# Optimization experiments

Measured on AMD Instinct MI355X. Metric: run time of the kernel, lower is better.

The kernel has to match this reference:

```python
import jax, jax.numpy as jnp
import numpy as np

N_NODES = 100000
N_EDGES = 1600000
IN_FEATS = 128
HID = 128
OUT_FEATS = 64


def setup_inputs() -> dict:
    key = jax.random.key(0)
    ks = jax.random.split(key, 8)
    node_ids = jnp.arange(N_NODES, dtype=jnp.int64)
    src = jax.random.randint(ks[0], (N_EDGES,), 0, N_NODES, dtype=jnp.int64)
    dst = jax.random.randint(ks[1], (N_EDGES,), 0, N_NODES, dtype=jnp.int64)
    emb = jax.random.normal(ks[2], (N_NODES, IN_FEATS), dtype=jnp.float32)
    W1 = jax.random.normal(ks[3], (IN_FEATS, HID), dtype=jnp.float32) / np.sqrt(IN_FEATS)
    b1 = jnp.zeros((HID,), dtype=jnp.float32)
    W2 = jax.random.normal(ks[4], (HID, OUT_FEATS), dtype=jnp.float32) / np.sqrt(HID)
    b2 = jnp.zeros((OUT_FEATS,), dtype=jnp.float32)
    return {"node_ids": node_ids, "src": src, "dst": dst, "emb": emb,
            "W1": W1, "b1": b1, "W2": W2, "b2": b2}


def _sym_norms(src, dst):
    # DGL GraphConv norm='both': D_out^{-1/2} on source side, D_in^{-1/2} on dest side,
    # degrees clamped to >= 1.
    ones = jnp.ones(src.shape[0], dtype=jnp.float32)
    deg_out = jax.ops.segment_sum(ones, src, num_segments=N_NODES)
    deg_in = jax.ops.segment_sum(ones, dst, num_segments=N_NODES)
    norm_src = jnp.clip(deg_out, 1.0, None) ** -0.5  # [N]
    norm_dst = jnp.clip(deg_in, 1.0, None) ** -0.5   # [N]
    return norm_src, norm_dst


def _spmm(src, dst, h):
    # rst[dst] += h[src]  (sparse adjacency aggregation)
    return jax.ops.segment_sum(h[src], dst, num_segments=N_NODES)


def reference(node_ids, src, dst, emb, W1, b1, W2, b2):
    norm_src, norm_dst = _sym_norms(src, dst)
    h = emb[node_ids]                                   # [N, IN]
    # Layer 1 (IN -> HID, relu): weight applied after aggregation (in <= out)
    h = _spmm(src, dst, h * norm_src[:, None]) * norm_dst[:, None]
    h = jax.nn.relu(h @ W1 + b1)                        # [N, HID]
    # Dropout(0.5) is identity in eval mode.
    # Layer 2 (HID -> OUT): DGL applies weight BEFORE aggregation when in > out
    h = (h @ W2) * norm_src[:, None]                    # [N, OUT]
    h = _spmm(src, dst, h) * norm_dst[:, None] + b2
    return h
```

## Files before the change

kernel.cpp:

```cpp
#include <hip/hip_runtime.h>

#define N_N 100000
#define N_E 1600000
#define SLOTS 48
#define N_PAD 100096

#define BK_SHIFT 8
#define BK_SIZE 256
#define NBKT 391
#define MAXB 5120
#define EPB2 4096
#define NBLK2 ((N_E + EPB2 - 1) / EPB2)
#define EPT 16

#define EMBB 6250
#define WB 96

typedef unsigned short ushort_t;
typedef unsigned int uint_t;
typedef _Float16 f16x8 __attribute__((ext_vector_type(8)));
typedef float f32x4 __attribute__((ext_vector_type(4)));

__device__ __forceinline__ ushort_t f2h(float f) {
    union { _Float16 h; ushort_t u; } c; c.h = (_Float16)f; return c.u;
}

__device__ __forceinline__ void acc2h(uint_t v, float wv, float& a, float& b) {
    union { uint_t u; _Float16 h[2]; } c; c.u = v;
    a = fmaf((float)c.h[0], wv, a);
    b = fmaf((float)c.h[1], wv, b);
}

__device__ __forceinline__ void addh(uint_t v, float& a, float& b) {
    union { uint_t u; _Float16 h[2]; } c; c.u = v;
    a += (float)c.h[0];
    b += (float)c.h[1];
}

__device__ __forceinline__ uint_t packh2(float a, float b) {
    union { _Float16 h[2]; uint_t u; } p;
    p.h[0] = (_Float16)a; p.h[1] = (_Float16)b;
    return p.u;
}

__global__ void __launch_bounds__(256) k_scatter_prep(
        const int* __restrict__ src, const int* __restrict__ dst,
        int* __restrict__ cur_d, int* __restrict__ cur_s,
        uint_t* __restrict__ pe_dst, uint_t* __restrict__ pe_src,
        const float* __restrict__ emb, ushort_t* __restrict__ embf,
        const float* __restrict__ W1, const float* __restrict__ W2,
        ushort_t* __restrict__ w1f, ushort_t* __restrict__ w2f) {
    int t = threadIdx.x, blk = blockIdx.x;
    if (blk >= NBLK2) {
        int pb = blk - NBLK2;
        if (pb < EMBB) {
            int i = pb * 512 + t;
            const float4* E4 = (const float4*)emb;
            ushort4* O4 = (ushort4*)embf;
            float4 v0 = E4[i], v1 = E4[i + 256];
            ushort4 o0, o1;
            o0.x = f2h(v0.x); o0.y = f2h(v0.y); o0.z = f2h(v0.z); o0.w = f2h(v0.w);
            o1.x = f2h(v1.x); o1.y = f2h(v1.y); o1.z = f2h(v1.z); o1.w = f2h(v1.w);
            O4[i] = o0; O4[i + 256] = o1;
        } else {
            int idx = (pb - EMBB) * 256 + t;
            int j = idx & 7, l = (idx >> 3) & 63;
            int k = (l >> 4) * 8 + j;
            int n = l & 15;
            if (idx < 16384) {
                int kc = (idx >> 9) & 3, nt = idx >> 11;
                w1f[idx] = f2h(W1[(kc * 32 + k) * 128 + nt * 16 + n]);
            } else {
                int i2 = idx - 16384;
                int kc = (i2 >> 9) & 3, nt = i2 >> 11;
                w2f[i2] = f2h(W2[(kc * 32 + k) * 64 + nt * 16 + n]);
            }
        }
        return;
    }
    __shared__ int cnt_[NBKT], lb_[NBKT], gb_[NBKT], cur_[NBKT];
    __shared__ int ps[512];
    __shared__ uint_t rec[EPB2];
    int e0 = blk * EPB2;
    for (int side = 0; side < 2; side++) {
        const int* key = side ? src : dst;
        for (int i = t; i < NBKT; i += 256) { cnt_[i] = 0; cur_[i] = 0; }
        __syncthreads();
        for (int i = 0; i < EPT; i++) {
            int e = e0 + t + i * 256;
            if (e < N_E) atomicAdd(&cnt_[key[e] >> BK_SHIFT], 1);
        }
        __syncthreads();
        ps[t] = (t < NBKT) ? cnt_[t] : 0;
        ps[t + 256] = (t + 256 < NBKT) ? cnt_[t + 256] : 0;
        __syncthreads();
        for (int d = 1; d < 512; d <<= 1) {
            int v0 = (t >= d) ? ps[t - d] : 0;
            int v1 = ps[t + 256 - d];
            __syncthreads();
            ps[t] += v0; ps[t + 256] += v1;
            __syncthreads();
        }
        int* curg = side ? cur_s : cur_d;
        for (int b = t; b < NBKT; b += 256) {
            int c = cnt_[b];
            lb_[b] = ps[b] - c;
            gb_[b] = c ? atomicAdd(&curg[b], c) : 0;
        }
        __syncthreads();
        for (int i = 0; i < EPT; i++) {
            int e = e0 + t + i * 256;
            if (e < N_E) {
                int s = src[e];
                int k = side ? s : dst[e];
                int b = k >> BK_SHIFT;
                int p = atomicAdd(&cur_[b], 1);
                rec[lb_[b] + p] = side ? (uint_t)s
                                       : ((uint_t)s | ((uint_t)(k & 255) << 17));
            }
        }
        __syncthreads();
        uint_t* pe = side ? pe_src : pe_dst;
        int wv = t >> 6, ln = t & 63, sub = ln >> 4, lj = ln & 15;
        for (int b0 = wv * 4; b0 < NBKT; b0 += 16) {
            int b = b0 + sub;
            if (b < NBKT) {
                int c = cnt_[b], lb = lb_[b], gb = gb_[b];
                for (int j = lj; j < c; j += 16)
                    if (gb + j < MAXB) pe[(size_t)b * MAXB + gb + j] = rec[lb + j];
            }
        }
        __syncthreads();
    }
}

__global__ void __launch_bounds__(512) k_binC(
        const uint_t* __restrict__ pe_dst, const uint_t* __restrict__ pe_src,
        const int* __restrict__ cur_d, const int* __restrict__ cur_s,
        int* __restrict__ slots, int* __restrict__ cnt,
        float* __restrict__ nd, float* __restrict__ ns) {
    int t = threadIdx.x, bb = blockIdx.x;
    __shared__ int lc[BK_SIZE];
    __shared__ int sslot[BK_SIZE * SLOTS];
    for (int i = t; i < BK_SIZE; i += 512) lc[i] = 0;
    __syncthreads();
    if (bb < NBKT) {
        int b = bb;
        int cb = min(cur_d[b], MAXB);
        int nbase = b << BK_SHIFT;
        const uint_t* pe = pe_dst + (size_t)b * MAXB;
        for (int e = t; e < cb; e += 512) {
            uint_t ed = pe[e];
            int dloc = (int)(ed >> 17);
            int s = (int)(ed & 0x1ffffu);
            int pos = atomicAdd(&lc[dloc], 1);
            if (pos < SLOTS) sslot[dloc * SLOTS + pos] = s;
        }
        __syncthreads();
        const uint4* S4 = (const uint4*)sslot;
        uint4* G4 = (uint4*)(slots + (size_t)nbase * SLOTS);
        for (int i = t; i < BK_SIZE * SLOTS / 4; i += 512) G4[i] = S4[i];
        for (int i = t; i < BK_SIZE; i += 512) {
            int n = nbase + i;
            if (n < N_N) {
                int c = lc[i];
                cnt[n] = c;
                nd[n] = 1.0f / sqrtf((float)max(c, 1));
            }
        }
    } else {
        int b = bb - NBKT;
        int cb = min(cur_s[b], MAXB);
        int nbase = b << BK_SHIFT;
        const uint_t* pe = pe_src + (size_t)b * MAXB;
        for (int e = t; e < cb; e += 512)
            atomicAdd(&lc[(int)pe[e] - nbase], 1);
        __syncthreads();
        for (int i = t; i < BK_SIZE; i += 512) {
            int n = nbase + i;
            if (n < N_N) ns[n] = 1.0f / sqrtf((float)max(lc[i], 1));
        }
    }
}

__global__ void __launch_bounds__(256) k_spmm1(
        const int* __restrict__ cnt, const int* __restrict__ slots,
        const ushort_t* __restrict__ embf, const float* __restrict__ ns,
        const float* __restrict__ nd, uint_t* __restrict__ aggf) {
    int wid = (blockIdx.x * 256 + (int)threadIdx.x) >> 6;
    int node = __builtin_amdgcn_readfirstlane(wid);
    if (node >= N_N) return;
    int lane = threadIdx.x & 63;
    const int* row = slots + (size_t)node * SLOTS;
    int len = min(cnt[node], SLOTS);
    float ax0 = 0.f, ay0 = 0.f, ax1 = 0.f, ay1 = 0.f;
    int e = 0;
    int n8 = len & ~7;
    for (; e < n8; e += 8) {
        int s0 = __builtin_amdgcn_readfirstlane(row[e + 0]);
        int s1 = __builtin_amdgcn_readfirstlane(row[e + 1]);
        int s2 = __builtin_amdgcn_readfirstlane(row[e + 2]);
        int s3 = __builtin_amdgcn_readfirstlane(row[e + 3]);
        int s4 = __builtin_amdgcn_readfirstlane(row[e + 4]);
        int s5 = __builtin_amdgcn_readfirstlane(row[e + 5]);
        int s6 = __builtin_amdgcn_readfirstlane(row[e + 6]);
        int s7 = __builtin_amdgcn_readfirstlane(row[e + 7]);
        float w0 = ns[s0], w1 = ns[s1], w2 = ns[s2], w3 = ns[s3];
        float w4 = ns[s4], w5 = ns[s5], w6 = ns[s6], w7 = ns[s7];
        uint_t v0 = ((const uint_t*)(embf + (size_t)s0 * 128))[lane];
        uint_t v1 = ((const uint_t*)(embf + (size_t)s1 * 128))[lane];
        uint_t v2 = ((const uint_t*)(embf + (size_t)s2 * 128))[lane];
        uint_t v3 = ((const uint_t*)(embf + (size_t)s3 * 128))[lane];
        uint_t v4 = ((const uint_t*)(embf + (size_t)s4 * 128))[lane];
        uint_t v5 = ((const uint_t*)(embf + (size_t)s5 * 128))[lane];
        uint_t v6 = ((const uint_t*)(embf + (size_t)s6 * 128))[lane];
        uint_t v7 = ((const uint_t*)(embf + (size_t)s7 * 128))[lane];
        acc2h(v0, w0, ax0, ay0);
        acc2h(v1, w1, ax1, ay1);
        acc2h(v2, w2, ax0, ay0);
        acc2h(v3, w3, ax1, ay1);
        acc2h(v4, w4, ax0, ay0);
        acc2h(v5, w5, ax1, ay1);
        acc2h(v6, w6, ax0, ay0);
        acc2h(v7, w7, ax1, ay1);
    }
    int n4 = len & ~3;
    for (; e < n4; e += 4) {
        int s0 = __builtin_amdgcn_readfirstlane(row[e + 0]);
        int s1 = __builtin_amdgcn_readfirstlane(row[e + 1]);
        int s2 = __builtin_amdgcn_readfirstlane(row[e + 2]);
        int s3 = __builtin_amdgcn_readfirstlane(row[e + 3]);
        float w0 = ns[s0], w1 = ns[s1], w2 = ns[s2], w3 = ns[s3];
        uint_t v0 = ((const uint_t*)(embf + (size_t)s0 * 128))[lane];
        uint_t v1 = ((const uint_t*)(embf + (size_t)s1 * 128))[lane];
        uint_t v2 = ((const uint_t*)(embf + (size_t)s2 * 128))[lane];
        uint_t v3 = ((const uint_t*)(embf + (size_t)s3 * 128))[lane];
        acc2h(v0, w0, ax0, ay0);
        acc2h(v1, w1, ax1, ay1);
        acc2h(v2, w2, ax0, ay0);
        acc2h(v3, w3, ax1, ay1);
    }
    for (; e < len; ++e) {
        int s = __builtin_amdgcn_readfirstlane(row[e]);
        float w = ns[s];
        uint_t v = ((const uint_t*)(embf + (size_t)s * 128))[lane];
        acc2h(v, w, ax0, ay0);
    }
    float sc = nd[node];
    aggf[(size_t)node * 64 + lane] = packh2((ax0 + ax1) * sc, (ay0 + ay1) * sc);
}

#define HSTH 136
__global__ void __launch_bounds__(256) k_gemm(
        const ushort_t* __restrict__ aggf, const ushort_t* __restrict__ w1f,
        const float* __restrict__ b1, const ushort_t* __restrict__ w2f,
        const float* __restrict__ ns, ushort_t* __restrict__ h2b) {
    __shared__ ushort_t w1s[16384];
    __shared__ ushort_t w2s[8192];
    __shared__ ushort_t sh[64 * HSTH];
    int t = threadIdx.x;
    int w = t >> 6, l = t & 63;
    int quad = l >> 4, lm = l & 15;
    int nb0 = blockIdx.x * 64;

    {
        uint4* d1 = (uint4*)w1s; const uint4* g1 = (const uint4*)w1f;
        for (int i = t; i < 2048; i += 256) d1[i] = g1[i];
        uint4* d2 = (uint4*)w2s; const uint4* g2 = (const uint4*)w2f;
        for (int i = t; i < 1024; i += 256) d2[i] = g2[i];
    }

    f16x8 a[4];
#pragma unroll
    for (int kc = 0; kc < 4; kc++)
        a[kc] = *(const f16x8*)(aggf
            + (size_t)(nb0 + w * 16 + lm) * 128 + kc * 32 + quad * 8);
    __syncthreads();

    f32x4 acc[8];
#pragma unroll
    for (int nt = 0; nt < 8; nt++) acc[nt] = (f32x4){0.f, 0.f, 0.f, 0.f};
#pragma unroll
    for (int kc = 0; kc < 4; kc++) {
        f16x8 bq[8];
#pragma unroll
        for (int nt = 0; nt < 8; nt++)
            bq[nt] = *(const f16x8*)(w1s + (((nt * 4 + kc) * 64 + l) << 3));
#pragma unroll
        for (int nt = 0; nt < 8; nt++)
            acc[nt] = __builtin_amdgcn_mfma_f32_16x16x32_f16(a[kc], bq[nt], acc[nt], 0, 0, 0);
    }
#pragma unroll
    for (int nt = 0; nt < 8; nt++) {
        float bb = b1[nt * 16 + lm];
#pragma unroll
        for (int r = 0; r < 4; r++) {
            int row = w * 16 + quad * 4 + r;
            sh[row * HSTH + nt * 16 + lm] = f2h(fmaxf(acc[nt][r] + bb, 0.f));
        }
    }
    __syncthreads();

    f16x8 hh[4];
#pragma unroll
    for (int kc = 0; kc < 4; kc++)
        hh[kc] = *(const f16x8*)(sh + (w * 16 + lm) * HSTH + kc * 32 + quad * 8);

    f32x4 acc2[4];
#pragma unroll
    for (int q = 0; q < 4; q++) acc2[q] = (f32x4){0.f, 0.f, 0.f, 0.f};
#pragma unroll
    for (int kc = 0; kc < 4; kc++) {
        f16x8 b2q[4];
#pragma unroll
        for (int q = 0; q < 4; q++)
            b2q[q] = *(const f16x8*)(w2s + (((q * 4 + kc) * 64 + l) << 3));
#pragma unroll
        for (int q = 0; q < 4; q++)
            acc2[q] = __builtin_amdgcn_mfma_f32_16x16x32_f16(hh[kc], b2q[q], acc2[q], 0, 0, 0);
    }
#pragma unroll
    for (int r = 0; r < 4; r++) {
        int node = nb0 + w * 16 + quad * 4 + r;
        if (node < N_N) {
            float s = ns[node];
#pragma unroll
            for (int q = 0; q < 4; q++)
                h2b[(size_t)node * 64 + q * 16 + lm] = f2h(acc2[q][r] * s);
        }
    }
}

__global__ void __launch_bounds__(256) k_spmm2(
        const int* __restrict__ cnt, const int* __restrict__ slots,
        const ushort_t* __restrict__ h2b, const float* __restrict__ nd,
        const float* __restrict__ b2, float* __restrict__ out) {
    int wid = (blockIdx.x * 256 + (int)threadIdx.x) >> 6;
    int node = __builtin_amdgcn_readfirstlane(wid);
    if (node >= N_N) return;
    int lane = threadIdx.x & 63;
    int q = lane >> 4, w16 = lane & 15;
    const int* row = slots + (size_t)node * SLOTS;
    int len = min(cnt[node], SLOTS);
    const uint2* H2 = (const uint2*)h2b;
    float a0 = 0.f, a1 = 0.f, a2 = 0.f, a3 = 0.f;
    int e = 0;
    int n16 = len & ~15;
    for (; e < n16; e += 16) {
        const int* rp = row + e + q;
        int s0 = rp[0], s1 = rp[4], s2 = rp[8], s3 = rp[12];
        uint2 v0 = H2[(size_t)s0 * 16 + w16];
        uint2 v1 = H2[(size_t)s1 * 16 + w16];
        uint2 v2 = H2[(size_t)s2 * 16 + w16];
        uint2 v3 = H2[(size_t)s3 * 16 + w16];
        addh(v0.x, a0, a1); addh(v0.y, a2, a3);
        addh(v1.x, a0, a1); addh(v1.y, a2, a3);
        addh(v2.x, a0, a1); addh(v2.y, a2, a3);
        addh(v3.x, a0, a1); addh(v3.y, a2, a3);
    }
    int n4 = len & ~3;
    for (; e < n4; e += 4) {
        int s = row[e + q];
        uint2 v = H2[(size_t)s * 16 + w16];
        addh(v.x, a0, a1); addh(v.y, a2, a3);
    }
    if (e < len && q < len - e) {
        int s = row[e + q];
        uint2 v = H2[(size_t)s * 16 + w16];
        addh(v.x, a0, a1); addh(v.y, a2, a3);
    }
    a0 += __shfl_xor(a0, 16); a1 += __shfl_xor(a1, 16);
    a2 += __shfl_xor(a2, 16); a3 += __shfl_xor(a3, 16);
    a0 += __shfl_xor(a0, 32); a1 += __shfl_xor(a1, 32);
    a2 += __shfl_xor(a2, 32); a3 += __shfl_xor(a3, 32);
    if (q == 0) {
        float sc = nd[node];
        float4 bb = ((const float4*)b2)[w16];
        float4 o;
        o.x = a0 * sc + bb.x;
        o.y = a1 * sc + bb.y;
        o.z = a2 * sc + bb.z;
        o.w = a3 * sc + bb.w;
        ((float4*)(out + (size_t)node * 64))[w16] = o;
    }
}

extern "C" void kernel_launch(void* const* d_in, const int* in_sizes, int n_in,
                              void* d_out, int out_size, void* d_ws, size_t ws_size,
                              hipStream_t stream) {
    const int* src = (const int*)d_in[1];
    const int* dst = (const int*)d_in[2];
    const float* emb = (const float*)d_in[3];
    const float* W1 = (const float*)d_in[4];
    const float* b1 = (const float*)d_in[5];
    const float* W2 = (const float*)d_in[6];
    const float* b2 = (const float*)d_in[7];
    float* out = (float*)d_out;

    int* cur_d   = (int*)d_ws;
    int* cur_s   = cur_d + 512;
    int* cnt     = cur_s + 512;
    float* ns    = (float*)(cnt + N_PAD);
    float* nd    = ns + N_PAD;
    int* slots   = (int*)(nd + N_PAD);
    uint_t* pe_dst = (uint_t*)(slots + (size_t)N_PAD * SLOTS);
    uint_t* pe_src = pe_dst + (size_t)NBKT * MAXB;
    ushort_t* embf = (ushort_t*)(pe_src + (size_t)NBKT * MAXB);
    uint_t* aggf = (uint_t*)(embf + (size_t)N_PAD * 128);
    ushort_t* w1f = (ushort_t*)(aggf + (size_t)N_PAD * 64);
    ushort_t* w2f = w1f + 16384;
    ushort_t* h2b = w2f + 8192;

    hipMemsetAsync(cur_d, 0, sizeof(int) * 1024, stream);
    k_scatter_prep<<<NBLK2 + EMBB + WB, 256, 0, stream>>>(
        src, dst, cur_d, cur_s, pe_dst, pe_src, emb, embf, W1, W2, w1f, w2f);
    k_binC  <<<2 * NBKT, 512, 0, stream>>>(
        pe_dst, pe_src, cur_d, cur_s, slots, cnt, nd, ns);
    k_spmm1 <<<(N_N + 3) / 4, 256, 0, stream>>>(cnt, slots, embf, ns, nd, aggf);
    k_gemm  <<<N_PAD / 64, 256, 0, stream>>>((const ushort_t*)aggf, w1f, b1, w2f, ns, h2b);
    k_spmm2 <<<(N_N + 3) / 4, 256, 0, stream>>>(cnt, slots, h2b, nd, b2, out);
}
```

Baseline: 285.1 us.

## Fuse first-layer SpMM gather into the MFMA GEMM kernel through shared memory

Merges the layer-1 neighbor aggregation and the two dense MFMA layers into one kernel. Each wave gathers 16 destination rows into an LDS tile, and the block then runs both GEMMs on that tile. This removes the fp16 aggregate buffer's global write and reread, plus one kernel launch. The weight fragments are now read straight from global memory instead of being staged in LDS. The grid shrinks from one wave per node to 64 nodes per block, which cuts the parallelism available to hide the random-gather latency.

```diff
diff --git a/kernel.cpp b/kernel.cpp
--- a/kernel.cpp
+++ b/kernel.cpp
@@ -183,113 +183,111 @@
     }
 }
 
-__global__ void __launch_bounds__(256) k_spmm1(
+#define HSTH 136
+__global__ void __launch_bounds__(256, 5) k_spmm1g(
         const int* __restrict__ cnt, const int* __restrict__ slots,
         const ushort_t* __restrict__ embf, const float* __restrict__ ns,
-        const float* __restrict__ nd, uint_t* __restrict__ aggf) {
-    int wid = (blockIdx.x * 256 + (int)threadIdx.x) >> 6;
-    int node = __builtin_amdgcn_readfirstlane(wid);
-    if (node >= N_N) return;
-    int lane = threadIdx.x & 63;
-    const int* row = slots + (size_t)node * SLOTS;
-    int len = min(cnt[node], SLOTS);
-    float ax0 = 0.f, ay0 = 0.f, ax1 = 0.f, ay1 = 0.f;
-    int e = 0;
-    int n8 = len & ~7;
-    for (; e < n8; e += 8) {
-        int s0 = __builtin_amdgcn_readfirstlane(row[e + 0]);
-        int s1 = __builtin_amdgcn_readfirstlane(row[e + 1]);
-        int s2 = __builtin_amdgcn_readfirstlane(row[e + 2]);
-        int s3 = __builtin_amdgcn_readfirstlane(row[e + 3]);
-        int s4 = __builtin_amdgcn_readfirstlane(row[e + 4]);
-        int s5 = __builtin_amdgcn_readfirstlane(row[e + 5]);
-        int s6 = __builtin_amdgcn_readfirstlane(row[e + 6]);
-        int s7 = __builtin_amdgcn_readfirstlane(row[e + 7]);
-        float w0 = ns[s0], w1 = ns[s1], w2 = ns[s2], w3 = ns[s3];
-        float w4 = ns[s4], w5 = ns[s5], w6 = ns[s6], w7 = ns[s7];
-        uint_t v0 = ((const uint_t*)(embf + (size_t)s0 * 128))[lane];
-        uint_t v1 = ((const uint_t*)(embf + (size_t)s1 * 128))[lane];
-        uint_t v2 = ((const uint_t*)(embf + (size_t)s2 * 128))[lane];
-        uint_t v3 = ((const uint_t*)(embf + (size_t)s3 * 128))[lane];
-        uint_t v4 = ((const uint_t*)(embf + (size_t)s4 * 128))[lane];
-        uint_t v5 = ((const uint_t*)(embf + (size_t)s5 * 128))[lane];
-        uint_t v6 = ((const uint_t*)(embf + (size_t)s6 * 128))[lane];
-        uint_t v7 = ((const uint_t*)(embf + (size_t)s7 * 128))[lane];
-        acc2h(v0, w0, ax0, ay0);
-        acc2h(v1, w1, ax1, ay1);
-        acc2h(v2, w2, ax0, ay0);
-        acc2h(v3, w3, ax1, ay1);
-        acc2h(v4, w4, ax0, ay0);
-        acc2h(v5, w5, ax1, ay1);
-        acc2h(v6, w6, ax0, ay0);
-        acc2h(v7, w7, ax1, ay1);
-    }
-    int n4 = len & ~3;
-    for (; e < n4; e += 4) {
-        int s0 = __builtin_amdgcn_readfirstlane(row[e + 0]);
-        int s1 = __builtin_amdgcn_readfirstlane(row[e + 1]);
-        int s2 = __builtin_amdgcn_readfirstlane(row[e + 2]);
-        int s3 = __builtin_amdgcn_readfirstlane(row[e + 3]);
-        float w0 = ns[s0], w1 = ns[s1], w2 = ns[s2], w3 = ns[s3];
-        uint_t v0 = ((const uint_t*)(embf + (size_t)s0 * 128))[lane];
-        uint_t v1 = ((const uint_t*)(embf + (size_t)s1 * 128))[lane];
-        uint_t v2 = ((const uint_t*)(embf + (size_t)s2 * 128))[lane];
-        uint_t v3 = ((const uint_t*)(embf + (size_t)s3 * 128))[lane];
-        acc2h(v0, w0, ax0, ay0);
-        acc2h(v1, w1, ax1, ay1);
-        acc2h(v2, w2, ax0, ay0);
-        acc2h(v3, w3, ax1, ay1);
-    }
-    for (; e < len; ++e) {
-        int s = __builtin_amdgcn_readfirstlane(row[e]);
-        float w = ns[s];
-        uint_t v = ((const uint_t*)(embf + (size_t)s * 128))[lane];
-        acc2h(v, w, ax0, ay0);
-    }
-    float sc = nd[node];
-    aggf[(size_t)node * 64 + lane] = packh2((ax0 + ax1) * sc, (ay0 + ay1) * sc);
-}
-
-#define HSTH 136
-__global__ void __launch_bounds__(256) k_gemm(
-        const ushort_t* __restrict__ aggf, const ushort_t* __restrict__ w1f,
-        const float* __restrict__ b1, const ushort_t* __restrict__ w2f,
-        const float* __restrict__ ns, ushort_t* __restrict__ h2b) {
-    __shared__ ushort_t w1s[16384];
-    __shared__ ushort_t w2s[8192];
+        const float* __restrict__ nd,
+        const ushort_t* __restrict__ w1f, const float* __restrict__ b1,
+        const ushort_t* __restrict__ w2f, ushort_t* __restrict__ h2b) {
     __shared__ ushort_t sh[64 * HSTH];
     int t = threadIdx.x;
-    int w = t >> 6, l = t & 63;
-    int quad = l >> 4, lm = l & 15;
+    int w = t >> 6, lane = t & 63;
+    int quad = lane >> 4, lm = lane & 15;
     int nb0 = blockIdx.x * 64;
 
-    {
-        uint4* d1 = (uint4*)w1s; const uint4* g1 = (const uint4*)w1f;
-        for (int i = t; i < 2048; i += 256) d1[i] = g1[i];
-        uint4* d2 = (uint4*)w2s; const uint4* g2 = (const uint4*)w2f;
-        for (int i = t; i < 1024; i += 256) d2[i] = g2[i];
-    }
+    for (int i = 0; i < 16; i++) {
+        int ri = w * 16 + i;
+        int node = nb0 + ri;
+        float ax0 = 0.f, ay0 = 0.f, ax1 = 0.f, ay1 = 0.f;
+        float sc = 0.f;
+        if (node < N_N) {
+            const int* row = slots + (size_t)node * SLOTS;
+            int len = min(cnt[node], SLOTS);
+            int e = 0;
+            int n8 = len & ~7;
+            for (; e < n8; e += 8) {
+                int s0 = __builtin_amdgcn_readfirstlane(row[e + 0]);
+                int s1 = __builtin_amdgcn_readfirstlane(row[e + 1]);
+                int s2 = __builtin_amdgcn_readfirstlane(row[e + 2]);
+                int s3 = __builtin_amdgcn_readfirstlane(row[e + 3]);
+                int s4 = __builtin_amdgcn_readfirstlane(row[e + 4]);
+                int s5 = __builtin_amdgcn_readfirstlane(row[e + 5]);
+                int s6 = __builtin_amdgcn_readfirstlane(row[e + 6]);
+                int s7 = __builtin_amdgcn_readfirstlane(row[e + 7]);
+                float w0 = ns[s0], w1 = ns[s1], w2 = ns[s2], w3 = ns[s3];
+                float w4 = ns[s4], w5 = ns[s5], w6 = ns[s6], w7 = ns[s7];
+                uint_t v0 = ((const uint_t*)(embf + (size_t)s0 * 128))[lane];
+                uint_t v1 = ((const uint_t*)(embf + (size_t)s1 * 128))[lane];
+                uint_t v2 = ((const uint_t*)(embf + (size_t)s2 * 128))[lane];
+                uint_t v3 = ((const uint_t*)(embf + (size_t)s3 * 128))[lane];
+                uint_t v4 = ((const uint_t*)(embf + (size_t)s4 * 128))[lane];
+                uint_t v5 = ((const uint_t*)(embf + (size_t)s5 * 128))[lane];
+                uint_t v6 = ((const uint_t*)(embf + (size_t)s6 * 128))[lane];
+                uint_t v7 = ((const uint_t*)(embf + (size_t)s7 * 128))[lane];
+                acc2h(v0, w0, ax0, ay0);
+                acc2h(v1, w1, ax1, ay1);
+                acc2h(v2, w2, ax0, ay0);
+                acc2h(v3, w3, ax1, ay1);
+                acc2h(v4, w4, ax0, ay0);
+                acc2h(v5, w5, ax1, ay1);
+                acc2h(v6, w6, ax0, ay0);
+                acc2h(v7, w7, ax1, ay1);
+            }
+            int n4 = len & ~3;
+            for (; e < n4; e += 4) {
+                int s0 = __builtin_amdgcn_readfirstlane(row[e + 0]);
+                int s1 = __builtin_amdgcn_readfirstlane(row[e + 1]);
+                int s2 = __builtin_amdgcn_readfirstlane(row[e + 2]);
+                int s3 = __builtin_amdgcn_readfirstlane(row[e + 3]);
+                float w0 = ns[s0], w1 = ns[s1], w2 = ns[s2], w3 = ns[s3];
+                uint_t v0 = ((const uint_t*)(embf + (size_t)s0 * 128))[lane];
+                uint_t v1 = ((const uint_t*)(embf + (size_t)s1 * 128))[lane];
+                uint_t v2 = ((const uint_t*)(embf + (size_t)s2 * 128))[lane];
+                uint_t v3 = ((const uint_t*)(embf + (size_t)s3 * 128))[lane];
+                acc2h(v0, w0, ax0, ay0);
+                acc2h(v1, w1, ax1, ay1);
+                acc2h(v2, w2, ax0, ay0);
+                acc2h(v3, w3, ax1, ay1);
+            }
+            for (; e < len; ++e) {
+                int s = __builtin_amdgcn_readfirstlane(row[e]);
+                float wv = ns[s];
+                uint_t v = ((const uint_t*)(embf + (size_t)s * 128))[lane];
+                acc2h(v, wv, ax0, ay0);
+            }
+            sc = nd[node];
+        }
+        *(uint_t*)(sh + ri * HSTH + 2 * lane) =
+            packh2((ax0 + ax1) * sc, (ay0 + ay1) * sc);
+    }
+    __syncthreads();
 
     f16x8 a[4];
 #pragma unroll
     for (int kc = 0; kc < 4; kc++)
-        a[kc] = *(const f16x8*)(aggf
-            + (size_t)(nb0 + w * 16 + lm) * 128 + kc * 32 + quad * 8);
+        a[kc] = *(const f16x8*)(sh + (w * 16 + lm) * HSTH + kc * 32 + quad * 8);
+
+    f32x4 acc[8];
+#pragma unroll
+    for (int nt = 0; nt < 8; nt++) acc[nt] = (f32x4){0.f, 0.f, 0.f, 0.f};
+#pragma unroll
+    for (int kc = 0; kc < 4; kc++) {
+#pragma unroll
+        for (int h = 0; h < 2; h++) {
+            f16x8 bq[4];
+#pragma unroll
+            for (int q = 0; q < 4; q++) {
+                int fp = (h * 4 + q) * 4 + kc;
+                bq[q] = *(const f16x8*)(w1f + ((fp * 64 + lane) << 3));
+            }
+#pragma unroll
+            for (int q = 0; q < 4; q++)
+                acc[h * 4 + q] = __builtin_amdgcn_mfma_f32_16x16x32_f16(
+                    a[kc], bq[q], acc[h * 4 + q], 0, 0, 0);
+        }
+    }
     __syncthreads();
-
-    f32x4 acc[8];
-#pragma unroll
-    for (int nt = 0; nt < 8; nt++) acc[nt] = (f32x4){0.f, 0.f, 0.f, 0.f};
-#pragma unroll
-    for (int kc = 0; kc < 4; kc++) {
-        f16x8 bq[8];
-#pragma unroll
-        for (int nt = 0; nt < 8; nt++)
-            bq[nt] = *(const f16x8*)(w1s + (((nt * 4 + kc) * 64 + l) << 3));
-#pragma unroll
-        for (int nt = 0; nt < 8; nt++)
-            acc[nt] = __builtin_amdgcn_mfma_f32_16x16x32_f16(a[kc], bq[nt], acc[nt], 0, 0, 0);
-    }
 #pragma unroll
     for (int nt = 0; nt < 8; nt++) {
         float bb = b1[nt * 16 + lm];
@@ -314,7 +312,7 @@
         f16x8 b2q[4];
 #pragma unroll
         for (int q = 0; q < 4; q++)
-            b2q[q] = *(const f16x8*)(w2s + (((q * 4 + kc) * 64 + l) << 3));
+            b2q[q] = *(const f16x8*)(w2f + (((q * 4 + kc) * 64 + lane) << 3));
 #pragma unroll
         for (int q = 0; q < 4; q++)
             acc2[q] = __builtin_amdgcn_mfma_f32_16x16x32_f16(hh[kc], b2q[q], acc2[q], 0, 0, 0);
@@ -406,8 +404,7 @@
     uint_t* pe_dst = (uint_t*)(slots + (size_t)N_PAD * SLOTS);
     uint_t* pe_src = pe_dst + (size_t)NBKT * MAXB;
     ushort_t* embf = (ushort_t*)(pe_src + (size_t)NBKT * MAXB);
-    uint_t* aggf = (uint_t*)(embf + (size_t)N_PAD * 128);
-    ushort_t* w1f = (ushort_t*)(aggf + (size_t)N_PAD * 64);
+    ushort_t* w1f = embf + (size_t)N_PAD * 128;
     ushort_t* w2f = w1f + 16384;
     ushort_t* h2b = w2f + 8192;
 
@@ -416,7 +413,7 @@
         src, dst, cur_d, cur_s, pe_dst, pe_src, emb, embf, W1, W2, w1f, w2f);
     k_binC  <<<2 * NBKT, 512, 0, stream>>>(
         pe_dst, pe_src, cur_d, cur_s, slots, cnt, nd, ns);
-    k_spmm1 <<<(N_N + 3) / 4, 256, 0, stream>>>(cnt, slots, embf, ns, nd, aggf);
-    k_gemm  <<<N_PAD / 64, 256, 0, stream>>>((const ushort_t*)aggf, w1f, b1, w2f, ns, h2b);
+    k_spmm1g<<<N_PAD / 64, 256, 0, stream>>>(
+        cnt, slots, embf, ns, nd, w1f, b1, w2f, h2b);
     k_spmm2 <<<(N_N + 3) / 4, 256, 0, stream>>>(cnt, slots, h2b, nd, b2, out);
 }
```

Result: slower. 323.7 us (+13.5%).

## Map one lane per output feature in layer-2 SpMM and halve scatter block size

Applied to the files above, without the earlier changes.

Layer-2 aggregation is rewritten so that each of the 64 lanes owns one output feature. Source indices are read as wave-uniform scalars and each neighbor row is fetched as 64 contiguous fp16 values, which removes the quad split, the cross-lane shuffle reduction and the predicated store. In exchange each lane issues narrow 2-byte loads instead of 8-byte vector loads, so more memory instructions are issued. The scatter-prep kernel also halves edges per block and edges per thread, giving more, smaller blocks.

```diff
diff --git a/kernel.cpp b/kernel.cpp
--- a/kernel.cpp
+++ b/kernel.cpp
@@ -9,9 +9,9 @@
 #define BK_SIZE 256
 #define NBKT 391
 #define MAXB 5120
-#define EPB2 4096
+#define EPB2 2048
 #define NBLK2 ((N_E + EPB2 - 1) / EPB2)
-#define EPT 16
+#define EPT 8
 
 #define EMBB 6250
 #define WB 96
@@ -25,16 +25,14 @@
     union { _Float16 h; ushort_t u; } c; c.h = (_Float16)f; return c.u;
 }
 
+__device__ __forceinline__ float h2f(ushort_t u) {
+    union { ushort_t u; _Float16 h; } c; c.u = u; return (float)c.h;
+}
+
 __device__ __forceinline__ void acc2h(uint_t v, float wv, float& a, float& b) {
     union { uint_t u; _Float16 h[2]; } c; c.u = v;
     a = fmaf((float)c.h[0], wv, a);
     b = fmaf((float)c.h[1], wv, b);
-}
-
-__device__ __forceinline__ void addh(uint_t v, float& a, float& b) {
-    union { uint_t u; _Float16 h[2]; } c; c.u = v;
-    a += (float)c.h[0];
-    b += (float)c.h[1];
 }
 
 __device__ __forceinline__ uint_t packh2(float a, float b) {
@@ -339,50 +337,51 @@
     int node = __builtin_amdgcn_readfirstlane(wid);
     if (node >= N_N) return;
     int lane = threadIdx.x & 63;
-    int q = lane >> 4, w16 = lane & 15;
     const int* row = slots + (size_t)node * SLOTS;
     int len = min(cnt[node], SLOTS);
-    const uint2* H2 = (const uint2*)h2b;
-    float a0 = 0.f, a1 = 0.f, a2 = 0.f, a3 = 0.f;
+    float a0 = 0.f, a1 = 0.f;
     int e = 0;
-    int n16 = len & ~15;
-    for (; e < n16; e += 16) {
-        const int* rp = row + e + q;
-        int s0 = rp[0], s1 = rp[4], s2 = rp[8], s3 = rp[12];
-        uint2 v0 = H2[(size_t)s0 * 16 + w16];
-        uint2 v1 = H2[(size_t)s1 * 16 + w16];
-        uint2 v2 = H2[(size_t)s2 * 16 + w16];
-        uint2 v3 = H2[(size_t)s3 * 16 + w16];
-        addh(v0.x, a0, a1); addh(v0.y, a2, a3);
-        addh(v1.x, a0, a1); addh(v1.y, a2, a3);
-        addh(v2.x, a0, a1); addh(v2.y, a2, a3);
-        addh(v3.x, a0, a1); addh(v3.y, a2, a3);
+    int n8 = len & ~7;
+    for (; e < n8; e += 8) {
+        int s0 = __builtin_amdgcn_readfirstlane(row[e + 0]);
+        int s1 = __builtin_amdgcn_readfirstlane(row[e + 1]);
+        int s2 = __builtin_amdgcn_readfirstlane(row[e + 2]);
+        int s3 = __builtin_amdgcn_readfirstlane(row[e + 3]);
+        int s4 = __builtin_amdgcn_readfirstlane(row[e + 4]);
+        int s5 = __builtin_amdgcn_readfirstlane(row[e + 5]);
+        int s6 = __builtin_amdgcn_readfirstlane(row[e + 6]);
+        int s7 = __builtin_amdgcn_readfirstlane(row[e + 7]);
+        ushort_t v0 = (h2b + (size_t)s0 * 64)[lane];
+        ushort_t v1 = (h2b + (size_t)s1 * 64)[lane];
+        ushort_t v2 = (h2b + (size_t)s2 * 64)[lane];
+        ushort_t v3 = (h2b + (size_t)s3 * 64)[lane];
+        ushort_t v4 = (h2b + (size_t)s4 * 64)[lane];
+        ushort_t v5 = (h2b + (size_t)s5 * 64)[lane];
+        ushort_t v6 = (h2b + (size_t)s6 * 64)[lane];
+        ushort_t v7 = (h2b + (size_t)s7 * 64)[lane];
+        a0 += h2f(v0); a1 += h2f(v1);
+        a0 += h2f(v2); a1 += h2f(v3);
+        a0 += h2f(v4); a1 += h2f(v5);
+        a0 += h2f(v6); a1 += h2f(v7);
     }
     int n4 = len & ~3;
     for (; e < n4; e += 4) {
-        int s = row[e + q];
-        uint2 v = H2[(size_t)s * 16 + w16];
-        addh(v.x, a0, a1); addh(v.y, a2, a3);
-    }
-    if (e < len && q < len - e) {
-        int s = row[e + q];
-        uint2 v = H2[(size_t)s * 16 + w16];
-        addh(v.x, a0, a1); addh(v.y, a2, a3);
-    }
-    a0 += __shfl_xor(a0, 16); a1 += __shfl_xor(a1, 16);
-    a2 += __shfl_xor(a2, 16); a3 += __shfl_xor(a3, 16);
-    a0 += __shfl_xor(a0, 32); a1 += __shfl_xor(a1, 32);
-    a2 += __shfl_xor(a2, 32); a3 += __shfl_xor(a3, 32);
-    if (q == 0) {
-        float sc = nd[node];
-        float4 bb = ((const float4*)b2)[w16];
-        float4 o;
-        o.x = a0 * sc + bb.x;
-        o.y = a1 * sc + bb.y;
-        o.z = a2 * sc + bb.z;
-        o.w = a3 * sc + bb.w;
-        ((float4*)(out + (size_t)node * 64))[w16] = o;
-    }
+        int s0 = __builtin_amdgcn_readfirstlane(row[e + 0]);
+        int s1 = __builtin_amdgcn_readfirstlane(row[e + 1]);
+        int s2 = __builtin_amdgcn_readfirstlane(row[e + 2]);
+        int s3 = __builtin_amdgcn_readfirstlane(row[e + 3]);
+        ushort_t v0 = (h2b + (size_t)s0 * 64)[lane];
+        ushort_t v1 = (h2b + (size_t)s1 * 64)[lane];
+        ushort_t v2 = (h2b + (size_t)s2 * 64)[lane];
+        ushort_t v3 = (h2b + (size_t)s3 * 64)[lane];
+        a0 += h2f(v0); a1 += h2f(v1);
+        a0 += h2f(v2); a1 += h2f(v3);
+    }
+    for (; e < len; ++e) {
+        int s = __builtin_amdgcn_readfirstlane(row[e]);
+        a0 += h2f((h2b + (size_t)s * 64)[lane]);
+    }
+    out[(size_t)node * 64 + lane] = (a0 + a1) * nd[node] + b2[lane];
 }
 
 extern "C" void kernel_launch(void* const* d_in, const int* in_sizes, int n_in,
```

After: 286.6 us. No clear change (+0.5%).
